# Optimization experiments

Hardware: AMD Instinct MI355X
Metric: run time of the kernel (lower is better)

## Reference

```python
import jax, jax.numpy as jnp
import numpy as np

N, C, H, W = 64, 256, 56, 56
NDEMOG = 4
HS, WS = 28, 28  # height*rate, width*rate


def _nearest_upsample_2d(a, out_h, out_w):
    # matches torch F.interpolate(mode='nearest'): idx = floor(i * in/out)
    h, w = a.shape[-2], a.shape[-1]
    ih = (jnp.arange(out_h) * h) // out_h
    iw = (jnp.arange(out_w) * w) // out_w
    return a[..., ih[:, None], iw[None, :]]


def setup_inputs() -> dict:
    key = jax.random.key(0)
    k1, k2, k3, k4 = jax.random.split(key, 4)
    x = jax.random.normal(k1, (N, C, H, W), dtype=jnp.float32)
    demog_label = jax.random.randint(k2, (N,), 0, NDEMOG)
    # xavier-ish small init, repeated across demog groups as in the torch code
    att_channel = jax.random.normal(k3, (NDEMOG, 1, C, 1, 1), dtype=jnp.float32) * 0.1
    att_spatial = jax.random.normal(k4, (NDEMOG, 1, 1, HS, WS), dtype=jnp.float32) * 0.1
    return {"x": x, "demog_label": demog_label,
            "att_channel": att_channel, "att_spatial": att_spatial}


def reference(x, demog_label, att_channel, att_spatial):
    # soft channel attention: (D,1,C,1,1) -> sigmoid
    ac = jax.nn.sigmoid(att_channel)
    # soft spatial attention, nearest-upsampled to (D,1,1,H,W)
    asp = _nearest_upsample_2d(jax.nn.sigmoid(att_spatial), H, W)
    # gather per-sample attention maps by demographic label and apply:
    # y[n,c,h,w] = x[n,c,h,w] * ac[demog[n],c] * asp[demog[n],h,w]
    gate_c = ac[demog_label, 0]      # (N, C, 1, 1)
    gate_s = asp[demog_label, 0]     # (N, 1, H, W)
    y = x * gate_c * gate_s
    return (y, ac, asp)
```

## Files before the change

### kernel.cpp

```cpp
#include <hip/hip_runtime.h>
#include <math.h>

#define NB   64
#define CC   256
#define HH   56
#define WW   56
#define NDEM 4
#define HS   28
#define WS   28

#define HW        (HH * WW)
#define HW4       (HW / 4)
#define Y_ELEMS   (NB * CC * HH * WW)
#define AC_ELEMS  (NDEM * CC)
#define ASP_ELEMS (NDEM * HH * WW)

typedef float fvec4 __attribute__((ext_vector_type(4)));

__global__ void att_gates_kernel(const float* __restrict__ att_channel,
                                 const float* __restrict__ att_spatial,
                                 float* __restrict__ ac_out,
                                 float* __restrict__ asp_out)
{
    int i = blockIdx.x * blockDim.x + threadIdx.x;
    const int total = AC_ELEMS + ASP_ELEMS;
    if (i >= total) return;
    if (i < AC_ELEMS) {
        float v = att_channel[i];
        ac_out[i] = 1.0f / (1.0f + expf(-v));
    } else {
        int j = i - AC_ELEMS;
        int d = j / HW;
        int r = j - d * HW;
        int h = r / WW;
        int w = r - h * WW;
        float v = att_spatial[d * (HS * WS) + (h >> 1) * WS + (w >> 1)];
        asp_out[j] = 1.0f / (1.0f + expf(-v));
    }
}

__global__ __launch_bounds__(256) void att_apply_kernel(
    const fvec4* __restrict__ x,
    const int*   __restrict__ demog,
    const float* __restrict__ ac,
    const fvec4* __restrict__ asp4,
    fvec4*       __restrict__ y)
{
    const int plane = blockIdx.x;
    const int n     = plane >> 8;
    const int c     = plane & 255;
    const int d     = demog[n];
    const float gc  = ac[(d << 8) + c];

    const int t = threadIdx.x;
    const fvec4* __restrict__ xa = x + (size_t)plane * HW4;
    fvec4*       __restrict__ ya = y + (size_t)plane * HW4;
    const fvec4* __restrict__ ga = asp4 + d * HW4;

    fvec4 x0 = __builtin_nontemporal_load(&xa[t]);
    fvec4 x1 = __builtin_nontemporal_load(&xa[t + 256]);
    fvec4 x2 = __builtin_nontemporal_load(&xa[t + 512]);
    fvec4 g0 = ga[t];
    fvec4 g1 = ga[t + 256];
    fvec4 g2 = ga[t + 512];

    fvec4 y0 = x0 * gc * g0;
    fvec4 y1 = x1 * gc * g1;
    fvec4 y2 = x2 * gc * g2;

    __builtin_nontemporal_store(y0, &ya[t]);
    __builtin_nontemporal_store(y1, &ya[t + 256]);
    __builtin_nontemporal_store(y2, &ya[t + 512]);

    if (t < 16) {
        int p = 768 + t;
        fvec4 xv = __builtin_nontemporal_load(&xa[p]);
        fvec4 gv = ga[p];
        fvec4 yv = xv * gc * gv;
        __builtin_nontemporal_store(yv, &ya[p]);
    }
}

extern "C" void kernel_launch(void* const* d_in, const int* in_sizes, int n_in,
                              void* d_out, int out_size, void* d_ws, size_t ws_size,
                              hipStream_t stream) {
    const float* x           = (const float*)d_in[0];
    const int*   demog       = (const int*)d_in[1];
    const float* att_channel = (const float*)d_in[2];
    const float* att_spatial = (const float*)d_in[3];

    float* y_out   = (float*)d_out;
    float* ac_out  = y_out + Y_ELEMS;
    float* asp_out = y_out + Y_ELEMS + AC_ELEMS;

    {
        int total  = AC_ELEMS + ASP_ELEMS;
        int blocks = (total + 255) / 256;
        att_gates_kernel<<<blocks, 256, 0, stream>>>(att_channel, att_spatial,
                                                     ac_out, asp_out);
    }

    {
        int blocks = NB * CC;
        att_apply_kernel<<<blocks, 256, 0, stream>>>(
            (const fvec4*)x, demog, ac_out, (const fvec4*)asp_out,
            (float4*)nullptr == nullptr ? (fvec4*)y_out : (fvec4*)y_out);
    }
}
```

Baseline: 76.67 us.

## Fuse gate computation into apply kernel, recomputing sigmoids inline per plane

Merges the separate gate kernel and the apply kernel into one launch. Extra blocks write the ac/asp outputs, while plane blocks recompute the channel and spatial sigmoids directly from the raw 28x28 attention map instead of reading the upsampled gate tensor. This removes one kernel launch and the dependency between the two kernels. In exchange each plane redoes expf work.

```diff
diff --git a/kernel.cpp b/kernel.cpp
--- a/kernel.cpp
+++ b/kernel.cpp
@@ -14,59 +14,75 @@
 #define Y_ELEMS   (NB * CC * HH * WW)
 #define AC_ELEMS  (NDEM * CC)
 #define ASP_ELEMS (NDEM * HH * WW)
+#define PLANES    (NB * CC)
+#define GATE_BLOCKS ((AC_ELEMS + ASP_ELEMS + 255) / 256)
 
 typedef float fvec4 __attribute__((ext_vector_type(4)));
+typedef float fvec2 __attribute__((ext_vector_type(2)));
 
-__global__ void att_gates_kernel(const float* __restrict__ att_channel,
-                                 const float* __restrict__ att_spatial,
-                                 float* __restrict__ ac_out,
-                                 float* __restrict__ asp_out)
-{
-    int i = blockIdx.x * blockDim.x + threadIdx.x;
-    const int total = AC_ELEMS + ASP_ELEMS;
-    if (i >= total) return;
-    if (i < AC_ELEMS) {
-        float v = att_channel[i];
-        ac_out[i] = 1.0f / (1.0f + expf(-v));
-    } else {
-        int j = i - AC_ELEMS;
-        int d = j / HW;
-        int r = j - d * HW;
-        int h = r / WW;
-        int w = r - h * WW;
-        float v = att_spatial[d * (HS * WS) + (h >> 1) * WS + (w >> 1)];
-        asp_out[j] = 1.0f / (1.0f + expf(-v));
-    }
+__device__ __forceinline__ float sigmoidf_(float v) {
+    return 1.0f / (1.0f + expf(-v));
 }
 
-__global__ __launch_bounds__(256) void att_apply_kernel(
+__global__ __launch_bounds__(256) void att_fused_kernel(
     const fvec4* __restrict__ x,
     const int*   __restrict__ demog,
-    const float* __restrict__ ac,
-    const fvec4* __restrict__ asp4,
-    fvec4*       __restrict__ y)
+    const float* __restrict__ att_channel,
+    const float* __restrict__ att_spatial,
+    fvec4*       __restrict__ y,
+    float*       __restrict__ ac_out,
+    float*       __restrict__ asp_out)
 {
-    const int plane = blockIdx.x;
-    const int n     = plane >> 8;
-    const int c     = plane & 255;
-    const int d     = demog[n];
-    const float gc  = ac[(d << 8) + c];
+    const int b = blockIdx.x;
+    const int t = threadIdx.x;
 
-    const int t = threadIdx.x;
-    const fvec4* __restrict__ xa = x + (size_t)plane * HW4;
-    fvec4*       __restrict__ ya = y + (size_t)plane * HW4;
-    const fvec4* __restrict__ ga = asp4 + d * HW4;
+    if (b >= PLANES) {
+        int i = (b - PLANES) * 256 + t;
+        if (i < AC_ELEMS) {
+            ac_out[i] = sigmoidf_(att_channel[i]);
+        } else if (i < AC_ELEMS + ASP_ELEMS) {
+            int j = i - AC_ELEMS;
+            int d = j / HW;
+            int r = j - d * HW;
+            int h = r / WW;
+            int w = r - h * WW;
+            asp_out[j] = sigmoidf_(att_spatial[d * (HS * WS) + (h >> 1) * WS + (w >> 1)]);
+        }
+        return;
+    }
+
+    const int n = b >> 8;
+    const int c = b & 255;
+    const int d = demog[n];
+    const float gc = sigmoidf_(att_channel[(d << 8) + c]);
+
+    const fvec4* __restrict__ xa = x + (size_t)b * HW4;
+    fvec4*       __restrict__ ya = y + (size_t)b * HW4;
+    const float* __restrict__ sa = att_spatial + d * (HS * WS);
+
+    #define GATE(p, gv)                                                     \
+    {                                                                       \
+        int h_  = (p) / 14;                                                 \
+        int w4_ = (p) - h_ * 14;                                            \
+        fvec2 a_ = *reinterpret_cast<const fvec2*>(                         \
+                        &sa[(h_ >> 1) * WS + 2 * w4_]);                     \
+        float s0_ = sigmoidf_(a_.x) * gc;                                   \
+        float s1_ = sigmoidf_(a_.y) * gc;                                   \
+        gv.x = s0_; gv.y = s0_; gv.z = s1_; gv.w = s1_;                     \
+    }
 
     fvec4 x0 = __builtin_nontemporal_load(&xa[t]);
     fvec4 x1 = __builtin_nontemporal_load(&xa[t + 256]);
     fvec4 x2 = __builtin_nontemporal_load(&xa[t + 512]);
-    fvec4 g0 = ga[t];
-    fvec4 g1 = ga[t + 256];
-    fvec4 g2 = ga[t + 512];
 
-    fvec4 y0 = x0 * gc * g0;
-    fvec4 y1 = x1 * gc * g1;
-    fvec4 y2 = x2 * gc * g2;
+    fvec4 g0, g1, g2;
+    GATE(t,       g0);
+    GATE(t + 256, g1);
+    GATE(t + 512, g2);
+
+    fvec4 y0 = x0 * g0;
+    fvec4 y1 = x1 * g1;
+    fvec4 y2 = x2 * g2;
 
     __builtin_nontemporal_store(y0, &ya[t]);
     __builtin_nontemporal_store(y1, &ya[t + 256]);
@@ -75,10 +91,12 @@
     if (t < 16) {
         int p = 768 + t;
         fvec4 xv = __builtin_nontemporal_load(&xa[p]);
-        fvec4 gv = ga[p];
-        fvec4 yv = xv * gc * gv;
+        fvec4 gv;
+        GATE(p, gv);
+        fvec4 yv = xv * gv;
         __builtin_nontemporal_store(yv, &ya[p]);
     }
+    #undef GATE
 }
 
 extern "C" void kernel_launch(void* const* d_in, const int* in_sizes, int n_in,
@@ -93,17 +111,8 @@
     float* ac_out  = y_out + Y_ELEMS;
     float* asp_out = y_out + Y_ELEMS + AC_ELEMS;
 
-    {
-        int total  = AC_ELEMS + ASP_ELEMS;
-        int blocks = (total + 255) / 256;
-        att_gates_kernel<<<blocks, 256, 0, stream>>>(att_channel, att_spatial,
-                                                     ac_out, asp_out);
-    }
-
-    {
-        int blocks = NB * CC;
-        att_apply_kernel<<<blocks, 256, 0, stream>>>(
-            (const fvec4*)x, demog, ac_out, (const fvec4*)asp_out,
-            (float4*)nullptr == nullptr ? (fvec4*)y_out : (fvec4*)y_out);
-    }
+    int blocks = PLANES + GATE_BLOCKS;
+    att_fused_kernel<<<blocks, 256, 0, stream>>>(
+        (const fvec4*)x, demog, att_channel, att_spatial,
+        (fvec4*)y_out, ac_out, asp_out);
 }
```

Result: faster. 69.59 us (-9.2%).
